# Kernel tuning notes

Measured on AMD Instinct MI355X. Metric: run time of the kernel, lower is better.

Reference implementation:

```python
import jax, jax.numpy as jnp
import numpy as np

B, LV, LS = 16, 512, 512
FEA_V, FEA_S = 2048, 768
D_MODEL, H, DK, DV = 1024, 16, 64, 64
EPS = 1e-6


def setup_inputs() -> dict:
    key = jax.random.key(0)
    ks = jax.random.split(key, 16)
    sc = lambda fan_in: 1.0 / np.sqrt(fan_in)
    return {
        "v": jax.random.normal(ks[0], (B, LV, FEA_V), jnp.float32),
        "s": jax.random.normal(ks[1], (B, LS, FEA_S), jnp.float32),
        "W_lv": jax.random.normal(ks[2], (FEA_V, D_MODEL), jnp.float32) * sc(FEA_V),
        "b_lv": jnp.zeros((D_MODEL,), jnp.float32),
        "W_ls": jax.random.normal(ks[3], (FEA_S, D_MODEL), jnp.float32) * sc(FEA_S),
        "b_ls": jnp.zeros((D_MODEL,), jnp.float32),
        "pos_v": jax.random.normal(ks[4], (1, LV, D_MODEL), jnp.float32),
        "pos_s": jax.random.normal(ks[5], (1, LS, D_MODEL), jnp.float32),
        "W_q": jax.random.normal(ks[6], (D_MODEL, H * DK), jnp.float32) * sc(D_MODEL),
        "b_q": jnp.zeros((H * DK,), jnp.float32),
        "W_k": jax.random.normal(ks[7], (D_MODEL, H * DK), jnp.float32) * sc(D_MODEL),
        "b_k": jnp.zeros((H * DK,), jnp.float32),
        "W_v": jax.random.normal(ks[8], (D_MODEL, H * DV), jnp.float32) * sc(D_MODEL),
        "b_v": jnp.zeros((H * DV,), jnp.float32),
        "W_p": jax.random.normal(ks[9], (H * DV, D_MODEL), jnp.float32) * sc(H * DV),
        "b_p": jnp.zeros((D_MODEL,), jnp.float32),
        "ln_gamma": jnp.ones((D_MODEL,), jnp.float32),
        "ln_beta": jnp.zeros((D_MODEL,), jnp.float32),
        "v_len": LV,
        "s_len": LS,
    }


def _layer_norm(x, gamma, beta):
    mu = jnp.mean(x, axis=-1, keepdims=True)
    var = jnp.var(x, axis=-1, keepdims=True)
    return gamma * (x - mu) / jnp.sqrt(var + EPS) + beta


def reference(v, s, W_lv, b_lv, W_ls, b_ls, pos_v, pos_s, W_q, b_q, W_k, b_k,
              W_v, b_v, W_p, b_p, ln_gamma, ln_beta, v_len, s_len):
    b_size = v.shape[0]
    # input projections + ReLU (dropout is identity at eval)
    v = jax.nn.relu(v @ W_lv + b_lv)  # [B, LV, D]
    s = jax.nn.relu(s @ W_ls + b_ls)  # [B, LS, D]
    # positional embedding add (pos=True)
    residual_v = v + pos_v[:, : v.shape[1], :]
    # QKV projections; note the original unpack `q_v, k_s, k_s = ...`
    # overwrites the key with the VALUE projection of s, so both key and
    # value in attention are v_s (the W_v projection of s). W_k output is
    # computed in torch but discarded.
    q = (v @ W_q + b_q).reshape(b_size, -1, H, DK).transpose(0, 2, 1, 3)   # [B,H,LV,DK]
    _k = (s @ W_k + b_k)  # computed then discarded, kept for faithfulness
    vs = (s @ W_v + b_v).reshape(b_size, -1, H, DV).transpose(0, 2, 1, 3)  # [B,H,LS,DV]
    scores = jnp.einsum("bhqd,bhkd->bhqk", q, vs) / jnp.sqrt(jnp.float32(DK))
    attn = jax.nn.softmax(scores, axis=-1)
    context = jnp.einsum("bhqk,bhkd->bhqd", attn, vs)  # [B,H,LV,DV]
    context = context.transpose(0, 2, 1, 3).reshape(b_size, -1, H * DV)
    output_v = context @ W_p + b_p  # dropout identity at eval
    return _layer_norm(residual_v + output_v, ln_gamma, ln_beta)
```

## Files before the change

### kernel.cpp

```cpp
#include <hip/hip_runtime.h>

typedef unsigned short u16;
typedef unsigned int   u32;

using bf16x8 = __attribute__((ext_vector_type(8))) short;
using f32x4  = __attribute__((ext_vector_type(4))) float;

#define MFMA16(a, b, c) __builtin_amdgcn_mfma_f32_16x16x32_bf16((a), (b), (c), 0, 0, 0)

__device__ __forceinline__ u16 f2bf(float f) {
  union { float f; u32 u; } x; x.f = f;
  u32 r = x.u + 0x7fffu + ((x.u >> 16) & 1u);
  return (u16)(r >> 16);
}

__device__ __forceinline__ float bf2f(u16 v) {
  union { u32 u; float f; } x; x.u = ((u32)v) << 16;
  return x.f;
}

__device__ __forceinline__ u32 cvtpk(float lo, float hi) {
  u32 r;
  asm("v_cvt_pk_bf16_f32 %0, %1, %2" : "=v"(r) : "v"(lo), "v"(hi));
  return r;
}

__device__ __forceinline__ void gl2lds16(const void* g, void* l) {
  __builtin_amdgcn_global_load_lds(
      (const __attribute__((address_space(1))) u32*)g,
      (__attribute__((address_space(3))) u32*)l, 16, 0, 0);
}

__global__ __launch_bounds__(256) void cvt_f32_bf16(const float* __restrict__ in,
                                                    u16* __restrict__ out, long n8) {
  long i = (long)blockIdx.x * 256 + threadIdx.x;
  if (i >= n8) return;
  const float4* p = (const float4*)(in + i * 8);
  float4 a = p[0], b = p[1];
  uint4 pk;
  pk.x = cvtpk(a.x, a.y);
  pk.y = cvtpk(a.z, a.w);
  pk.z = cvtpk(b.x, b.y);
  pk.w = cvtpk(b.z, b.w);
  *(uint4*)(out + i * 8) = pk;
}

__global__ __launch_bounds__(256) void wt_cvt_t(const float* __restrict__ W,
                                                u16* __restrict__ Wt, int K, int N) {
  __shared__ u16 t[64][66];
  int tilesN = N >> 6;
  int k0 = ((int)blockIdx.x / tilesN) << 6;
  int n0 = ((int)blockIdx.x % tilesN) << 6;
  int tid = threadIdx.x;
  int c4 = (tid & 15) * 4, r16 = tid >> 4;
#pragma unroll
  for (int p = 0; p < 4; ++p) {
    int row = r16 + p * 16;
    float4 f = *(const float4*)(W + (size_t)(k0 + row) * N + n0 + c4);
    t[row][c4 + 0] = f2bf(f.x);
    t[row][c4 + 1] = f2bf(f.y);
    t[row][c4 + 2] = f2bf(f.z);
    t[row][c4 + 3] = f2bf(f.w);
  }
  __syncthreads();
  int c8 = (tid & 7) * 8, r32 = tid >> 3;
#pragma unroll
  for (int p = 0; p < 2; ++p) {
    int n = r32 + p * 32;
    u16 tmp[8] __attribute__((aligned(16)));
#pragma unroll
    for (int e = 0; e < 8; ++e) tmp[e] = t[c8 + e][n];
    *(uint4*)(Wt + (size_t)(n0 + n) * K + k0 + c8) = *(uint4*)tmp;
  }
}

template <int MODE>
__global__ __launch_bounds__(512) void gemm_bf16(
    const u16* __restrict__ A, const u16* __restrict__ Bt,
    const float* __restrict__ bias, u16* __restrict__ outb, float* __restrict__ outf,
    u16* __restrict__ outt, const u16* __restrict__ add0b,
    const float* __restrict__ add1, int M, int N, int K) {
  __shared__ u16 sA[2][256 * 64];
  __shared__ u16 sB[2][128 * 64];
  int tilesN = N >> 7;
  int nwg = (int)gridDim.x;
  int cpx = nwg >> 3;
  int orig = (int)blockIdx.x;
  int wg = (orig & 7) * cpx + (orig >> 3);
  int tm = wg / tilesN, tn = wg % tilesN;
  int m0 = tm << 8, n0 = tn << 7;
  int tid = threadIdx.x, w = tid >> 6, l = tid & 63;
  int wm = (w >> 1) << 6, wn = (w & 1) << 6;
  int c16 = l & 15, hi = l >> 4, g16 = hi * 16;

  f32x4 acc[4][4];
#pragma unroll
  for (int i = 0; i < 4; ++i)
#pragma unroll
    for (int j = 0; j < 4; ++j) acc[i][j] = (f32x4){0.f, 0.f, 0.f, 0.f};

  auto STAGE = [&](int kt, int buf) {
    const u16* Ab = A + (size_t)m0 * K + kt * 64;
    const u16* Bb = Bt + (size_t)n0 * K + kt * 64;
#pragma unroll
    for (int p = 0; p < 4; ++p) {
      int lin = p * 8192 + tid * 16;
      int row = lin >> 7;
      int cb = (lin & 127) ^ ((row & 7) << 4);
      gl2lds16(Ab + (size_t)row * K + (cb >> 1), (char*)sA[buf] + (lin & ~1023));
    }
#pragma unroll
    for (int p = 0; p < 2; ++p) {
      int lin = p * 8192 + tid * 16;
      int row = lin >> 7;
      int cb = (lin & 127) ^ ((row & 7) << 4);
      gl2lds16(Bb + (size_t)row * K + (cb >> 1), (char*)sB[buf] + (lin & ~1023));
    }
  };

  auto COMPUTE = [&](int buf) {
#pragma unroll
    for (int kk = 0; kk < 2; ++kk) {
      bf16x8 af[4], bfr[4];
#pragma unroll
      for (int i = 0; i < 4; ++i) {
        int ar = wm + i * 16 + c16;
        af[i] = *(const bf16x8*)((const char*)sA[buf] + ar * 128 +
                                 ((kk * 64 + g16) ^ ((ar & 7) << 4)));
      }
#pragma unroll
      for (int j = 0; j < 4; ++j) {
        int br = wn + j * 16 + c16;
        bfr[j] = *(const bf16x8*)((const char*)sB[buf] + br * 128 +
                                  ((kk * 64 + g16) ^ ((br & 7) << 4)));
      }
#pragma unroll
      for (int i = 0; i < 4; ++i)
#pragma unroll
        for (int j = 0; j < 4; ++j) acc[i][j] = MFMA16(af[i], bfr[j], acc[i][j]);
    }
  };

  int nk = K >> 6;
  STAGE(0, 0);
  int cur = 0;
  for (int kt = 0; kt < nk; ++kt) {
    if (kt + 1 < nk) {
      STAGE(kt + 1, cur ^ 1);
      __builtin_amdgcn_sched_barrier(0);
      asm volatile("s_waitcnt vmcnt(6)" ::: "memory");
    } else {
      asm volatile("s_waitcnt vmcnt(0)" ::: "memory");
    }
    __builtin_amdgcn_s_barrier();
    __builtin_amdgcn_sched_barrier(0);
    COMPUTE(cur);
    __builtin_amdgcn_sched_barrier(0);
    __builtin_amdgcn_s_barrier();
    cur ^= 1;
  }

#pragma unroll
  for (int i = 0; i < 4; ++i) {
#pragma unroll
    for (int j = 0; j < 4; ++j) {
      float vv[4];
      int gn = n0 + wn + j * 16 + c16;
#pragma unroll
      for (int r = 0; r < 4; ++r) vv[r] = acc[i][j][r] + bias[gn];
      int gm0 = m0 + wm + i * 16 + hi * 4;
      if (MODE == 0) {
#pragma unroll
        for (int r = 0; r < 4; ++r)
          outb[(size_t)(gm0 + r) * N + gn] = f2bf(fmaxf(vv[r], 0.f));
      } else if (MODE == 2 || MODE == 4) {
        int hh = gn >> 6, dk = gn & 63, bb2 = gm0 >> 9, ll2 = gm0 & 511;
#pragma unroll
        for (int r = 0; r < 4; ++r)
          outb[(((size_t)bb2 * 16 + hh) * 512 + ll2 + r) * 64 + dk] = f2bf(vv[r]);
        if (MODE == 4) {
          uint2 tw;
          tw.x = cvtpk(vv[0], vv[1]);
          tw.y = cvtpk(vv[2], vv[3]);
          *(uint2*)(outt + (((size_t)bb2 * 16 + hh) * 64 + dk) * 512 + ll2) = tw;
        }
      } else {
#pragma unroll
        for (int r = 0; r < 4; ++r) {
          int gm = gm0 + r;
          float v = vv[r] + bf2f(add0b[(size_t)gm * N + gn]) +
                    add1[(size_t)(gm & 511) * N + gn];
          outf[(size_t)gm * N + gn] = v;
        }
      }
    }
  }
}

__global__ __launch_bounds__(512) void attn_kernel(const u16* __restrict__ q,
                                                   const u16* __restrict__ kv,
                                                   const u16* __restrict__ kvT,
                                                   u16* __restrict__ ctx) {
  __shared__ u16 sK[2][4096];
  __shared__ u16 sVT[2][4096];
  __shared__ u16 sP[8192];

  int orig = (int)blockIdx.x;
  int r = (orig & 7) * 128 + (orig >> 3);
  int bh = r >> 2, qt = r & 3;
  int b = bh >> 4, h = bh & 15;
  int tid = threadIdx.x, w = tid >> 6, l = tid & 63;
  int c16 = l & 15, hi = l >> 4, g16 = hi * 16;
  int swzq = (c16 & 7) << 4;

  const u16* qbase = q + (size_t)bh * 32768 + (size_t)qt * 8192;
#pragma unroll
  for (int j = 0; j < 2; ++j) {
    int chunk = w * 2 + j;
    int lin = chunk * 1024 + l * 16;
    int row = lin >> 7;
    int cb = (lin & 127) ^ ((row & 7) << 4);
    gl2lds16(qbase + (size_t)row * 64 + (cb >> 1), (char*)sP + chunk * 1024);
  }
  {
    const u16* kb = kv + (size_t)bh * 32768;
    const u16* vb = kvT + (size_t)bh * 32768;
    int lin = w * 1024 + l * 16;
    int row = lin >> 7;
    int cb = (lin & 127) ^ ((row & 7) << 4);
    gl2lds16(kb + (size_t)row * 64 + (cb >> 1), (char*)sK[0] + w * 1024);
    gl2lds16(vb + (size_t)row * 512 + (cb >> 1), (char*)sVT[0] + w * 1024);
  }
  __syncthreads();

  const char* sQrow = (const char*)sP + (w * 16 + c16) * 128;
  bf16x8 qf0 = *(const bf16x8*)(sQrow + ((0 + g16) ^ swzq));
  bf16x8 qf1 = *(const bf16x8*)(sQrow + ((64 + g16) ^ swzq));

  char* sPw = (char*)sP + w * 2048;
  f32x4 of[4];
#pragma unroll
  for (int n = 0; n < 4; ++n) of[n] = (f32x4){0.f, 0.f, 0.f, 0.f};
  float m_run = -1e30f, l_run = 0.f;

  for (int c = 0; c < 8; ++c) {
    int cur = c & 1;
    if (c < 7) {
      const u16* kb = kv + (size_t)bh * 32768 + (size_t)(c + 1) * 4096;
      const u16* vb = kvT + (size_t)bh * 32768 + (c + 1) * 64;
      int lin = w * 1024 + l * 16;
      int row = lin >> 7;
      int cb = (lin & 127) ^ ((row & 7) << 4);
      gl2lds16(kb + (size_t)row * 64 + (cb >> 1), (char*)sK[cur ^ 1] + w * 1024);
      gl2lds16(vb + (size_t)row * 512 + (cb >> 1), (char*)sVT[cur ^ 1] + w * 1024);
    }
    const char* kbuf = (const char*)sK[cur];
    const char* vtbuf = (const char*)sVT[cur];

    f32x4 sf[4];
#pragma unroll
    for (int n = 0; n < 4; ++n) {
      const char* krow = kbuf + (n * 16 + c16) * 128;
      bf16x8 k0 = *(const bf16x8*)(krow + (g16 ^ swzq));
      bf16x8 k1 = *(const bf16x8*)(krow + ((64 + g16) ^ swzq));
      f32x4 z = (f32x4){0.f, 0.f, 0.f, 0.f};
      z = MFMA16(k0, qf0, z);
      z = MFMA16(k1, qf1, z);
      sf[n] = z;
    }

    float pmax = -1e30f;
#pragma unroll
    for (int n = 0; n < 4; ++n)
#pragma unroll
      for (int rr = 0; rr < 4; ++rr) {
        sf[n][rr] *= 0.125f;
        pmax = fmaxf(pmax, sf[n][rr]);
      }
    pmax = fmaxf(pmax, __shfl_xor(pmax, 16));
    pmax = fmaxf(pmax, __shfl_xor(pmax, 32));
    float mnew = fmaxf(m_run, pmax);
    float corr = __expf(m_run - mnew);
    float psum = 0.f;
#pragma unroll
    for (int n = 0; n < 4; ++n)
#pragma unroll
      for (int rr = 0; rr < 4; ++rr) {
        float p = __expf(sf[n][rr] - mnew);
        sf[n][rr] = p;
        psum += p;
      }
    psum += __shfl_xor(psum, 16);
    psum += __shfl_xor(psum, 32);
    l_run = l_run * corr + psum;
    m_run = mnew;
#pragma unroll
    for (int n = 0; n < 4; ++n)
#pragma unroll
      for (int rr = 0; rr < 4; ++rr) of[n][rr] *= corr;

#pragma unroll
    for (int n = 0; n < 4; ++n) {
      uint2 pw;
      pw.x = cvtpk(sf[n][0], sf[n][1]);
      pw.y = cvtpk(sf[n][2], sf[n][3]);
      *(uint2*)(sPw + c16 * 128 + ((n * 32 + hi * 8) ^ swzq)) = pw;
    }

    bf16x8 pf0 = *(const bf16x8*)(sPw + c16 * 128 + (g16 ^ swzq));
    bf16x8 pf1 = *(const bf16x8*)(sPw + c16 * 128 + ((64 + g16) ^ swzq));
#pragma unroll
    for (int n = 0; n < 4; ++n) {
      const char* vrow = vtbuf + (n * 16 + c16) * 128;
      bf16x8 v0 = *(const bf16x8*)(vrow + (g16 ^ swzq));
      bf16x8 v1 = *(const bf16x8*)(vrow + ((64 + g16) ^ swzq));
      of[n] = MFMA16(v0, pf0, of[n]);
      of[n] = MFMA16(v1, pf1, of[n]);
    }
    __syncthreads();
  }

  float inv = 1.0f / l_run;
  int grow = qt * 128 + w * 16 + c16;
  u16* obase = ctx + (size_t)(b * 512 + grow) * 1024 + h * 64;
#pragma unroll
  for (int n = 0; n < 4; ++n) {
    uint2 ow;
    ow.x = cvtpk(of[n][0] * inv, of[n][1] * inv);
    ow.y = cvtpk(of[n][2] * inv, of[n][3] * inv);
    *(uint2*)(obase + n * 16 + hi * 4) = ow;
  }
}

__global__ __launch_bounds__(256) void ln_kernel(float* __restrict__ x,
                                                 const float* __restrict__ gamma,
                                                 const float* __restrict__ beta) {
  __shared__ float red[4];
  __shared__ float red2[4];
  int row = blockIdx.x, tid = threadIdx.x;
  float4 v = *(float4*)(x + (size_t)row * 1024 + tid * 4);
  float s = v.x + v.y + v.z + v.w;
#pragma unroll
  for (int d = 1; d < 64; d <<= 1) s += __shfl_xor(s, d);
  if ((tid & 63) == 0) red[tid >> 6] = s;
  __syncthreads();
  float mu = (red[0] + red[1] + red[2] + red[3]) * (1.0f / 1024.0f);
  float d0 = v.x - mu, d1 = v.y - mu, d2 = v.z - mu, d3 = v.w - mu;
  float qq = d0 * d0 + d1 * d1 + d2 * d2 + d3 * d3;
#pragma unroll
  for (int d = 1; d < 64; d <<= 1) qq += __shfl_xor(qq, d);
  if ((tid & 63) == 0) red2[tid >> 6] = qq;
  __syncthreads();
  float var = (red2[0] + red2[1] + red2[2] + red2[3]) * (1.0f / 1024.0f);
  float rstd = rsqrtf(var + 1e-6f);
  float4 g = *(const float4*)(gamma + tid * 4);
  float4 bb = *(const float4*)(beta + tid * 4);
  v.x = g.x * d0 * rstd + bb.x;
  v.y = g.y * d1 * rstd + bb.y;
  v.z = g.z * d2 * rstd + bb.z;
  v.w = g.w * d3 * rstd + bb.w;
  *(float4*)(x + (size_t)row * 1024 + tid * 4) = v;
}

extern "C" void kernel_launch(void* const* d_in, const int* in_sizes, int n_in,
                              void* d_out, int out_size, void* d_ws, size_t ws_size,
                              hipStream_t stream) {
  (void)in_sizes; (void)n_in; (void)out_size; (void)ws_size;
  const float* v_in  = (const float*)d_in[0];
  const float* s_in  = (const float*)d_in[1];
  const float* W_lv  = (const float*)d_in[2];
  const float* b_lv  = (const float*)d_in[3];
  const float* W_ls  = (const float*)d_in[4];
  const float* b_ls  = (const float*)d_in[5];
  const float* pos_v = (const float*)d_in[6];
  const float* W_q   = (const float*)d_in[8];
  const float* b_q   = (const float*)d_in[9];
  const float* W_v   = (const float*)d_in[12];
  const float* b_v   = (const float*)d_in[13];
  const float* W_p   = (const float*)d_in[14];
  const float* b_p   = (const float*)d_in[15];
  const float* gamma = (const float*)d_in[16];
  const float* beta  = (const float*)d_in[17];
  float* out = (float*)d_out;

  char* ws = (char*)d_ws;
  size_t off = 0;
  auto alloc = [&](size_t bytes) {
    char* p = ws + off;
    off += (bytes + 255) & ~(size_t)255;
    return p;
  };
  u16* v_bf     = (u16*)alloc(33554432);
  u16* s_bf     = (u16*)alloc(12582912);
  u16* Wlv_t    = (u16*)alloc(4194304);
  u16* Wls_t    = (u16*)alloc(1572864);
  u16* Wq_t     = (u16*)alloc(2097152);
  u16* Wv_t     = (u16*)alloc(2097152);
  u16* Wp_t     = (u16*)alloc(2097152);
  u16* vproj_bf = (u16*)alloc(16777216);
  u16* sproj_bf = (u16*)alloc(16777216);
  u16* q_bf     = (u16*)alloc(16777216);
  u16* vs_bf    = (u16*)alloc(16777216);
  u16* vsT_bf   = (u16*)alloc(16777216);
  u16* ctx_bf   = (u16*)alloc(16777216);

  cvt_f32_bf16<<<8192, 256, 0, stream>>>(v_in, v_bf, 2097152);
  cvt_f32_bf16<<<3072, 256, 0, stream>>>(s_in, s_bf, 786432);
  wt_cvt_t<<<512, 256, 0, stream>>>(W_lv, Wlv_t, 2048, 1024);
  wt_cvt_t<<<192, 256, 0, stream>>>(W_ls, Wls_t, 768, 1024);
  wt_cvt_t<<<256, 256, 0, stream>>>(W_q, Wq_t, 1024, 1024);
  wt_cvt_t<<<256, 256, 0, stream>>>(W_v, Wv_t, 1024, 1024);
  wt_cvt_t<<<256, 256, 0, stream>>>(W_p, Wp_t, 1024, 1024);

  gemm_bf16<0><<<256, 512, 0, stream>>>(v_bf, Wlv_t, b_lv, vproj_bf, nullptr,
                                        nullptr, nullptr, nullptr, 8192, 1024, 2048);
  gemm_bf16<0><<<256, 512, 0, stream>>>(s_bf, Wls_t, b_ls, sproj_bf, nullptr,
                                        nullptr, nullptr, nullptr, 8192, 1024, 768);
  gemm_bf16<2><<<256, 512, 0, stream>>>(vproj_bf, Wq_t, b_q, q_bf, nullptr,
                                        nullptr, nullptr, nullptr, 8192, 1024, 1024);
  gemm_bf16<4><<<256, 512, 0, stream>>>(sproj_bf, Wv_t, b_v, vs_bf, nullptr,
                                        vsT_bf, nullptr, nullptr, 8192, 1024, 1024);
  attn_kernel<<<1024, 512, 0, stream>>>(q_bf, vs_bf, vsT_bf, ctx_bf);
  gemm_bf16<3><<<256, 512, 0, stream>>>(ctx_bf, Wp_t, b_p, nullptr, out,
                                        nullptr, vproj_bf, pos_v, 8192, 1024, 1024);
  ln_kernel<<<8192, 256, 0, stream>>>(out, gamma, beta);
}
```

Before: 248.1 us.

## Shrink GEMM tile to 128x128 and triple-buffer A loads

The bf16 GEMM moves from 256x128 tiles with 512 threads to 128x128 tiles with 256 threads, doubling the grid to 512 workgroups. The A operand now uses a three-slot LDS ring prefetched two k-steps ahead, while B stays double-buffered one step ahead, with matching vmcnt waits. The aim is better CU occupancy and load balance across the 256 CUs, plus deeper latency hiding for A. The cost is more redundant B traffic per output and a more intricate prefetch schedule.

```diff
diff --git a/kernel.cpp b/kernel.cpp
--- a/kernel.cpp
+++ b/kernel.cpp
@@ -75,12 +75,12 @@
 }
 
 template <int MODE>
-__global__ __launch_bounds__(512) void gemm_bf16(
+__global__ __launch_bounds__(256) void gemm_bf16(
     const u16* __restrict__ A, const u16* __restrict__ Bt,
     const float* __restrict__ bias, u16* __restrict__ outb, float* __restrict__ outf,
     u16* __restrict__ outt, const u16* __restrict__ add0b,
     const float* __restrict__ add1, int M, int N, int K) {
-  __shared__ u16 sA[2][256 * 64];
+  __shared__ u16 sA[3][128 * 64];
   __shared__ u16 sB[2][128 * 64];
   int tilesN = N >> 7;
   int nwg = (int)gridDim.x;
@@ -88,7 +88,7 @@
   int orig = (int)blockIdx.x;
   int wg = (orig & 7) * cpx + (orig >> 3);
   int tm = wg / tilesN, tn = wg % tilesN;
-  int m0 = tm << 8, n0 = tn << 7;
+  int m0 = tm << 7, n0 = tn << 7;
   int tid = threadIdx.x, w = tid >> 6, l = tid & 63;
   int wm = (w >> 1) << 6, wn = (w & 1) << 6;
   int c16 = l & 15, hi = l >> 4, g16 = hi * 16;
@@ -99,40 +99,44 @@
 #pragma unroll
     for (int j = 0; j < 4; ++j) acc[i][j] = (f32x4){0.f, 0.f, 0.f, 0.f};
 
-  auto STAGE = [&](int kt, int buf) {
+  auto STAGE_A = [&](int kt, int slot) {
     const u16* Ab = A + (size_t)m0 * K + kt * 64;
-    const u16* Bb = Bt + (size_t)n0 * K + kt * 64;
 #pragma unroll
     for (int p = 0; p < 4; ++p) {
-      int lin = p * 8192 + tid * 16;
+      int lin = p * 4096 + tid * 16;
       int row = lin >> 7;
       int cb = (lin & 127) ^ ((row & 7) << 4);
-      gl2lds16(Ab + (size_t)row * K + (cb >> 1), (char*)sA[buf] + (lin & ~1023));
-    }
-#pragma unroll
-    for (int p = 0; p < 2; ++p) {
-      int lin = p * 8192 + tid * 16;
+      gl2lds16(Ab + (size_t)row * K + (cb >> 1),
+               (char*)sA + slot * 16384 + (lin & ~1023));
+    }
+  };
+  auto STAGE_B = [&](int kt, int slot) {
+    const u16* Bb = Bt + (size_t)n0 * K + kt * 64;
+#pragma unroll
+    for (int p = 0; p < 4; ++p) {
+      int lin = p * 4096 + tid * 16;
       int row = lin >> 7;
       int cb = (lin & 127) ^ ((row & 7) << 4);
-      gl2lds16(Bb + (size_t)row * K + (cb >> 1), (char*)sB[buf] + (lin & ~1023));
+      gl2lds16(Bb + (size_t)row * K + (cb >> 1),
+               (char*)sB + slot * 16384 + (lin & ~1023));
     }
   };
 
-  auto COMPUTE = [&](int buf) {
+  auto COMPUTE = [&](int aslot, int bslot) {
+    const char* ab = (const char*)sA + aslot * 16384;
+    const char* bb = (const char*)sB + bslot * 16384;
 #pragma unroll
     for (int kk = 0; kk < 2; ++kk) {
       bf16x8 af[4], bfr[4];
 #pragma unroll
       for (int i = 0; i < 4; ++i) {
         int ar = wm + i * 16 + c16;
-        af[i] = *(const bf16x8*)((const char*)sA[buf] + ar * 128 +
-                                 ((kk * 64 + g16) ^ ((ar & 7) << 4)));
+        af[i] = *(const bf16x8*)(ab + ar * 128 + ((kk * 64 + g16) ^ ((ar & 7) << 4)));
       }
 #pragma unroll
       for (int j = 0; j < 4; ++j) {
         int br = wn + j * 16 + c16;
-        bfr[j] = *(const bf16x8*)((const char*)sB[buf] + br * 128 +
-                                  ((kk * 64 + g16) ^ ((br & 7) << 4)));
+        bfr[j] = *(const bf16x8*)(bb + br * 128 + ((kk * 64 + g16) ^ ((br & 7) << 4)));
       }
 #pragma unroll
       for (int i = 0; i < 4; ++i)
@@ -142,22 +146,33 @@
   };
 
   int nk = K >> 6;
-  STAGE(0, 0);
-  int cur = 0;
+  STAGE_A(0, 0);
+  STAGE_B(0, 0);
+  STAGE_A(1, 1);
+  int ar = 0, br = 0;
+  int aw = 2, bw = 1;
   for (int kt = 0; kt < nk; ++kt) {
-    if (kt + 1 < nk) {
-      STAGE(kt + 1, cur ^ 1);
+    if (kt + 2 < nk) {
+      STAGE_A(kt + 2, aw);
+      STAGE_B(kt + 1, bw);
       __builtin_amdgcn_sched_barrier(0);
-      asm volatile("s_waitcnt vmcnt(6)" ::: "memory");
+      asm volatile("s_waitcnt vmcnt(8)" ::: "memory");
+    } else if (kt + 1 < nk) {
+      STAGE_B(kt + 1, bw);
+      __builtin_amdgcn_sched_barrier(0);
+      asm volatile("s_waitcnt vmcnt(4)" ::: "memory");
     } else {
       asm volatile("s_waitcnt vmcnt(0)" ::: "memory");
     }
     __builtin_amdgcn_s_barrier();
     __builtin_amdgcn_sched_barrier(0);
-    COMPUTE(cur);
+    COMPUTE(ar, br);
     __builtin_amdgcn_sched_barrier(0);
     __builtin_amdgcn_s_barrier();
-    cur ^= 1;
+    ar = (ar == 2) ? 0 : ar + 1;
+    aw = (aw == 2) ? 0 : aw + 1;
+    br ^= 1;
+    bw ^= 1;
   }
 
 #pragma unroll
@@ -412,16 +427,16 @@
   wt_cvt_t<<<256, 256, 0, stream>>>(W_v, Wv_t, 1024, 1024);
   wt_cvt_t<<<256, 256, 0, stream>>>(W_p, Wp_t, 1024, 1024);
 
-  gemm_bf16<0><<<256, 512, 0, stream>>>(v_bf, Wlv_t, b_lv, vproj_bf, nullptr,
+  gemm_bf16<0><<<512, 256, 0, stream>>>(v_bf, Wlv_t, b_lv, vproj_bf, nullptr,
                                         nullptr, nullptr, nullptr, 8192, 1024, 2048);
-  gemm_bf16<0><<<256, 512, 0, stream>>>(s_bf, Wls_t, b_ls, sproj_bf, nullptr,
+  gemm_bf16<0><<<512, 256, 0, stream>>>(s_bf, Wls_t, b_ls, sproj_bf, nullptr,
                                         nullptr, nullptr, nullptr, 8192, 1024, 768);
-  gemm_bf16<2><<<256, 512, 0, stream>>>(vproj_bf, Wq_t, b_q, q_bf, nullptr,
+  gemm_bf16<2><<<512, 256, 0, stream>>>(vproj_bf, Wq_t, b_q, q_bf, nullptr,
                                         nullptr, nullptr, nullptr, 8192, 1024, 1024);
-  gemm_bf16<4><<<256, 512, 0, stream>>>(sproj_bf, Wv_t, b_v, vs_bf, nullptr,
+  gemm_bf16<4><<<512, 256, 0, stream>>>(sproj_bf, Wv_t, b_v, vs_bf, nullptr,
                                         vsT_bf, nullptr, nullptr, 8192, 1024, 1024);
   attn_kernel<<<1024, 512, 0, stream>>>(q_bf, vs_bf, vsT_bf, ctx_bf);
-  gemm_bf16<3><<<256, 512, 0, stream>>>(ctx_bf, Wp_t, b_p, nullptr, out,
+  gemm_bf16<3><<<512, 256, 0, stream>>>(ctx_bf, Wp_t, b_p, nullptr, out,
                                         nullptr, vproj_bf, pos_v, 8192, 1024, 1024);
   ln_kernel<<<8192, 256, 0, stream>>>(out, gamma, beta);
 }
```

Result: faster. 228.2 us (-8.0%).

## Split GEMM main loop into two phases interleaving B/A staging with MFMA halves

Applied to the files above, without the earlier changes.

Restructures the double-buffered GEMM K-loop so the B tile for the next step is issued first and the A tile is issued mid-iteration. Each iteration now runs as two MFMA half-phases (columns 0-1, then 2-3), with LDS reads and global-to-LDS loads interleaved between them. s_setprio is raised around the MFMA blocks. The intent is to spread memory traffic across the compute and hide load latency, at the cost of extra barriers per iteration and more live registers.

```diff
diff --git a/kernel.cpp b/kernel.cpp
--- a/kernel.cpp
+++ b/kernel.cpp
@@ -99,9 +99,18 @@
 #pragma unroll
     for (int j = 0; j < 4; ++j) acc[i][j] = (f32x4){0.f, 0.f, 0.f, 0.f};
 
-  auto STAGE = [&](int kt, int buf) {
+  auto STAGE_B = [&](int kt, int buf) {
+    const u16* Bb = Bt + (size_t)n0 * K + kt * 64;
+#pragma unroll
+    for (int p = 0; p < 2; ++p) {
+      int lin = p * 8192 + tid * 16;
+      int row = lin >> 7;
+      int cb = (lin & 127) ^ ((row & 7) << 4);
+      gl2lds16(Bb + (size_t)row * K + (cb >> 1), (char*)sB[buf] + (lin & ~1023));
+    }
+  };
+  auto STAGE_A = [&](int kt, int buf) {
     const u16* Ab = A + (size_t)m0 * K + kt * 64;
-    const u16* Bb = Bt + (size_t)n0 * K + kt * 64;
 #pragma unroll
     for (int p = 0; p < 4; ++p) {
       int lin = p * 8192 + tid * 16;
@@ -109,54 +118,83 @@
       int cb = (lin & 127) ^ ((row & 7) << 4);
       gl2lds16(Ab + (size_t)row * K + (cb >> 1), (char*)sA[buf] + (lin & ~1023));
     }
-#pragma unroll
-    for (int p = 0; p < 2; ++p) {
-      int lin = p * 8192 + tid * 16;
-      int row = lin >> 7;
-      int cb = (lin & 127) ^ ((row & 7) << 4);
-      gl2lds16(Bb + (size_t)row * K + (cb >> 1), (char*)sB[buf] + (lin & ~1023));
-    }
   };
 
-  auto COMPUTE = [&](int buf) {
-#pragma unroll
-    for (int kk = 0; kk < 2; ++kk) {
-      bf16x8 af[4], bfr[4];
-#pragma unroll
-      for (int i = 0; i < 4; ++i) {
-        int ar = wm + i * 16 + c16;
-        af[i] = *(const bf16x8*)((const char*)sA[buf] + ar * 128 +
-                                 ((kk * 64 + g16) ^ ((ar & 7) << 4)));
-      }
-#pragma unroll
-      for (int j = 0; j < 4; ++j) {
-        int br = wn + j * 16 + c16;
-        bfr[j] = *(const bf16x8*)((const char*)sB[buf] + br * 128 +
-                                  ((kk * 64 + g16) ^ ((br & 7) << 4)));
-      }
-#pragma unroll
-      for (int i = 0; i < 4; ++i)
-#pragma unroll
-        for (int j = 0; j < 4; ++j) acc[i][j] = MFMA16(af[i], bfr[j], acc[i][j]);
-    }
-  };
-
   int nk = K >> 6;
-  STAGE(0, 0);
+  STAGE_B(0, 0);
+  STAGE_A(0, 0);
   int cur = 0;
   for (int kt = 0; kt < nk; ++kt) {
-    if (kt + 1 < nk) {
-      STAGE(kt + 1, cur ^ 1);
+    bool more = (kt + 1 < nk);
+    const char* ab = (const char*)sA[cur];
+    const char* bb = (const char*)sB[cur];
+    bf16x8 af[2][4];
+
+    if (more) STAGE_B(kt + 1, cur ^ 1);
+    __builtin_amdgcn_sched_barrier(0);
+    if (more) asm volatile("s_waitcnt vmcnt(2)" ::: "memory");
+    else      asm volatile("s_waitcnt vmcnt(0)" ::: "memory");
+    __builtin_amdgcn_s_barrier();
+    __builtin_amdgcn_sched_barrier(0);
+    {
+#pragma unroll
+      for (int kk = 0; kk < 2; ++kk)
+#pragma unroll
+        for (int i = 0; i < 4; ++i) {
+          int arr = wm + i * 16 + c16;
+          af[kk][i] = *(const bf16x8*)(ab + arr * 128 +
+                                       ((kk * 64 + g16) ^ ((arr & 7) << 4)));
+        }
+      bf16x8 bf01[2][2];
+#pragma unroll
+      for (int j = 0; j < 2; ++j) {
+        int brr = wn + j * 16 + c16;
+#pragma unroll
+        for (int kk = 0; kk < 2; ++kk)
+          bf01[kk][j] = *(const bf16x8*)(bb + brr * 128 +
+                                         ((kk * 64 + g16) ^ ((brr & 7) << 4)));
+      }
+      __builtin_amdgcn_s_setprio(1);
+#pragma unroll
+      for (int kk = 0; kk < 2; ++kk)
+#pragma unroll
+        for (int i = 0; i < 4; ++i)
+#pragma unroll
+          for (int j = 0; j < 2; ++j)
+            acc[i][j] = MFMA16(af[kk][i], bf01[kk][j], acc[i][j]);
+      __builtin_amdgcn_s_setprio(0);
+    }
+    __builtin_amdgcn_sched_barrier(0);
+    __builtin_amdgcn_s_barrier();
+    __builtin_amdgcn_sched_barrier(0);
+
+    {
+      bf16x8 bf23[2][2];
+#pragma unroll
+      for (int j = 0; j < 2; ++j) {
+        int brr = wn + (2 + j) * 16 + c16;
+#pragma unroll
+        for (int kk = 0; kk < 2; ++kk)
+          bf23[kk][j] = *(const bf16x8*)(bb + brr * 128 +
+                                         ((kk * 64 + g16) ^ ((brr & 7) << 4)));
+      }
+      if (more) STAGE_A(kt + 1, cur ^ 1);
       __builtin_amdgcn_sched_barrier(0);
-      asm volatile("s_waitcnt vmcnt(6)" ::: "memory");
-    } else {
-      asm volatile("s_waitcnt vmcnt(0)" ::: "memory");
-    }
+      __builtin_amdgcn_s_barrier();
+      __builtin_amdgcn_sched_barrier(0);
+      __builtin_amdgcn_s_setprio(1);
+#pragma unroll
+      for (int kk = 0; kk < 2; ++kk)
+#pragma unroll
+        for (int i = 0; i < 4; ++i)
+#pragma unroll
+          for (int j = 0; j < 2; ++j)
+            acc[i][2 + j] = MFMA16(af[kk][i], bf23[kk][j], acc[i][2 + j]);
+      __builtin_amdgcn_s_setprio(0);
+    }
+    __builtin_amdgcn_sched_barrier(0);
     __builtin_amdgcn_s_barrier();
     __builtin_amdgcn_sched_barrier(0);
-    COMPUTE(cur);
-    __builtin_amdgcn_sched_barrier(0);
-    __builtin_amdgcn_s_barrier();
     cur ^= 1;
   }
 
```

Result: faster. 241.2 us (-2.8%).
